# Kernel tuning notes

Hardware: AMD Instinct MI355X
Metric: run time of the kernel (lower is better)

Reference implementation:

```python
import jax, jax.numpy as jnp
import numpy as np

HIDDEN = 4096
NUM_HEADS = 32
NUM_KV_HEADS = 8
HEAD_DIM = HIDDEN // NUM_HEADS  # 128
GROUPS = NUM_HEADS // NUM_KV_HEADS  # 4
ROPE_THETA = 10000.0


def setup_inputs() -> dict:
    key = jax.random.key(0)
    ks = jax.random.split(key, 5)
    B, S = 1, 2048
    w_scale = 0.02
    hidden_states = jax.random.normal(ks[0], (B, S, HIDDEN), dtype=jnp.float32)
    # nn.Linear weights stored as [out_features, in_features] (torch convention)
    Wq = jax.random.normal(ks[1], (NUM_HEADS * HEAD_DIM, HIDDEN), dtype=jnp.float32) * w_scale
    Wk = jax.random.normal(ks[2], (NUM_KV_HEADS * HEAD_DIM, HIDDEN), dtype=jnp.float32) * w_scale
    Wv = jax.random.normal(ks[3], (NUM_KV_HEADS * HEAD_DIM, HIDDEN), dtype=jnp.float32) * w_scale
    Wo = jax.random.normal(ks[4], (HIDDEN, NUM_HEADS * HEAD_DIM), dtype=jnp.float32) * w_scale
    position_ids = jnp.arange(S, dtype=jnp.int32)[None, :]  # [B, S]
    return {"hidden_states": hidden_states, "Wq": Wq, "Wk": Wk, "Wv": Wv,
            "Wo": Wo, "position_ids": position_ids}


def _rotate_half(x):
    h = x.shape[-1] // 2
    return jnp.concatenate([-x[..., h:], x[..., :h]], axis=-1)


def _rope_cos_sin(position_ids, dtype):
    # Llama rotary embedding: inv_freq over even dims, duplicated halves.
    inv_freq = 1.0 / (ROPE_THETA ** (jnp.arange(0, HEAD_DIM, 2, dtype=jnp.float32) / HEAD_DIM))
    freqs = position_ids.astype(jnp.float32)[..., None] * inv_freq  # [B, S, HD/2]
    emb = jnp.concatenate([freqs, freqs], axis=-1)  # [B, S, HD]
    cos = jnp.cos(emb)[:, None].astype(dtype)  # [B, 1, S, HD]
    sin = jnp.sin(emb)[:, None].astype(dtype)
    return cos, sin


def reference(hidden_states, Wq, Wk, Wv, Wo, position_ids):
    B, S, _ = hidden_states.shape
    # q/k/v projections (no bias, attention_bias=False)
    q = (hidden_states @ Wq.T).reshape(B, S, NUM_HEADS, HEAD_DIM).transpose(0, 2, 1, 3)
    k = (hidden_states @ Wk.T).reshape(B, S, NUM_KV_HEADS, HEAD_DIM).transpose(0, 2, 1, 3)
    v = (hidden_states @ Wv.T).reshape(B, S, NUM_KV_HEADS, HEAD_DIM).transpose(0, 2, 1, 3)
    # RoPE
    cos, sin = _rope_cos_sin(position_ids, hidden_states.dtype)
    q = q * cos + _rotate_half(q) * sin
    k = k * cos + _rotate_half(k) * sin
    # repeat_kv for GQA
    k = jnp.repeat(k, GROUPS, axis=1)  # [B, NH, S, HD]
    v = jnp.repeat(v, GROUPS, axis=1)
    # causal scaled dot product attention (matches the module's custom SDPA helper)
    scale = jnp.asarray(1.0 / np.sqrt(HEAD_DIM), hidden_states.dtype)
    scores = jnp.einsum('bhqd,bhkd->bhqk', q, k) * scale
    causal = jnp.tril(jnp.ones((S, S), dtype=bool))
    scores = jnp.where(causal, scores, jnp.asarray(-1e9, scores.dtype))
    attn = jax.nn.softmax(scores, axis=-1)
    out = jnp.einsum('bhqk,bhkd->bhqd', attn, v)  # [B, NH, S, HD]
    out = out.transpose(0, 2, 1, 3).reshape(B, S, NUM_HEADS * HEAD_DIM)
    return out @ Wo.T
```

## Files before the change

### kernel.cpp

```cpp
#include <hip/hip_runtime.h>
#include <hip/hip_fp16.h>

#define S_LEN 2048
#define HID   4096
#define NH    32
#define NKV   8
#define HD    128

using half8 = __attribute__((ext_vector_type(8))) _Float16;
using f32x4 = __attribute__((ext_vector_type(4))) float;

__device__ __forceinline__ void async16(const void* g, void* l) {
  __builtin_amdgcn_global_load_lds(
      (const __attribute__((address_space(1))) unsigned int*)g,
      (__attribute__((address_space(3))) unsigned int*)l, 16, 0, 0);
}

__global__ void k_cvt(const float* __restrict__ in, __half* __restrict__ out, int n) {
  int idx = blockIdx.x * blockDim.x + threadIdx.x;
  int stride = gridDim.x * blockDim.x;
  for (int i = idx * 4; i < n; i += stride * 4) {
    float4 v = *(const float4*)(in + i);
    __half2* o = (__half2*)(out + i);
    o[0] = __floats2half2_rn(v.x, v.y);
    o[1] = __floats2half2_rn(v.z, v.w);
  }
}

__global__ __launch_bounds__(256) void k_gemm(const __half* __restrict__ A,
                                              const __half* __restrict__ B,
                                              __half* __restrict__ Ch,
                                              float* __restrict__ Cf,
                                              int M, int N, int K, int mode) {
  __shared__ __half As[128 * 32];
  __shared__ __half Bs[128 * 32];
  const int tid = threadIdx.x;
  const int lane = tid & 63;
  const int wave = tid >> 6;
  const int m0 = blockIdx.x * 128, n0 = blockIdx.y * 128;
  const int wm = (wave >> 1) * 64, wn = (wave & 1) * 64;
  const int lr = lane & 15, lg = lane >> 4;

  f32x4 acc[4][4];
#pragma unroll
  for (int i = 0; i < 4; ++i)
#pragma unroll
    for (int j = 0; j < 4; ++j) acc[i][j] = f32x4{0.f, 0.f, 0.f, 0.f};

  for (int kt = 0; kt < K; kt += 32) {
    __syncthreads();
#pragma unroll
    for (int q = 0; q < 2; ++q) {
      int chunk = q * 256 + wave * 64 + lane;
      int row = chunk >> 2, kc = chunk & 3;
      async16(A + (size_t)(m0 + row) * K + kt + kc * 8,
              (char*)As + q * 4096 + wave * 1024);
      async16(B + (size_t)(n0 + row) * K + kt + kc * 8,
              (char*)Bs + q * 4096 + wave * 1024);
    }
    __syncthreads();

    half8 af[4], bfr[4];
#pragma unroll
    for (int i = 0; i < 4; ++i) {
      af[i]  = *(const half8*)((const char*)As + (wm + i * 16 + lr) * 64 + lg * 16);
      bfr[i] = *(const half8*)((const char*)Bs + (wn + i * 16 + lr) * 64 + lg * 16);
    }
#pragma unroll
    for (int i = 0; i < 4; ++i)
#pragma unroll
      for (int j = 0; j < 4; ++j)
        acc[i][j] = __builtin_amdgcn_mfma_f32_16x16x32_f16(af[i], bfr[j], acc[i][j], 0, 0, 0);
  }

#pragma unroll
  for (int i = 0; i < 4; ++i)
#pragma unroll
    for (int j = 0; j < 4; ++j) {
      int col = n0 + wn + j * 16 + lr;
#pragma unroll
      for (int r = 0; r < 4; ++r) {
        int row = m0 + wm + i * 16 + lg * 4 + r;
        if (mode == 1)      Cf[(size_t)row * N + col] = acc[i][j][r];
        else if (mode == 2) Ch[(size_t)col * M + row] = __float2half(acc[i][j][r]);
        else                Ch[(size_t)row * N + col] = __float2half(acc[i][j][r]);
      }
    }
}

__global__ void k_rope(__half* __restrict__ Q, __half* __restrict__ Kv,
                       const int* __restrict__ pos) {
  int idx = blockIdx.x * blockDim.x + threadIdx.x;
  int j = idx & 63;
  int hh = (idx >> 6) % (NH + NKV);
  int s = idx / (64 * (NH + NKV));
  float p = (float)pos[s];
  float invf = exp2f(-(float)j * (13.287712379549449f / 64.0f));
  float ang = p * invf;
  float c, sn;
  sincosf(ang, &c, &sn);
  __half* base = (hh < NH) ? (Q + (size_t)s * HID + hh * HD)
                           : (Kv + (size_t)s * (NKV * HD) + (hh - NH) * HD);
  float x0 = __half2float(base[j]);
  float x1 = __half2float(base[j + 64]);
  base[j]      = __float2half(x0 * c + x1 * sn);
  base[j + 64] = __float2half(x1 * c - x0 * sn);
}

__global__ __launch_bounds__(256) void k_attn(const __half* __restrict__ Q,
                                              const __half* __restrict__ K,
                                              const __half* __restrict__ Vt,
                                              __half* __restrict__ O) {
  __shared__ char Ks[64 * 256];
  __shared__ char Vs[128 * 128];
  __shared__ char Ps[4][2048];
  const int tid = threadIdx.x, lane = tid & 63, wave = tid >> 6;
  const int qb = blockIdx.x, h = blockIdx.y;
  const int kvh = h >> 2;
  const int q0 = qb * 64 + wave * 16;
  const int lr = lane & 15, lg = lane >> 4;

  half8 qf[4];
#pragma unroll
  for (int kc = 0; kc < 4; ++kc)
    qf[kc] = *(const half8*)(Q + (size_t)(q0 + lr) * HID + h * HD + kc * 32 + lg * 8);

  float m_r[4], l_r[4];
  f32x4 oa[8];
#pragma unroll
  for (int r = 0; r < 4; ++r) { m_r[r] = -1e30f; l_r[r] = 0.f; }
#pragma unroll
  for (int t8 = 0; t8 < 8; ++t8) oa[t8] = f32x4{0.f, 0.f, 0.f, 0.f};

  const int kv_end = qb * 64 + 64;
  for (int kv0 = 0; kv0 < kv_end; kv0 += 64) {
    __syncthreads();
#pragma unroll
    for (int q = 0; q < 4; ++q) {
      int chunk = q * 256 + tid;
      int row = chunk >> 4, ck = chunk & 15;
      uint4 d = *(const uint4*)(K + (size_t)(kv0 + row) * (NKV * HD) + kvh * HD + ck * 8);
      *(uint4*)(Ks + row * 256 + (((ck ^ (row & 7))) << 4)) = d;
    }
#pragma unroll
    for (int q = 0; q < 4; ++q) {
      int chunk = q * 256 + tid;
      int row = chunk >> 3, ck = chunk & 7;
      uint4 d = *(const uint4*)(Vt + (size_t)(kvh * HD + row) * S_LEN + kv0 + ck * 8);
      *(uint4*)(Vs + row * 128 + (((ck ^ (row & 7))) << 4)) = d;
    }
    __syncthreads();

    f32x4 sc[4];
#pragma unroll
    for (int c = 0; c < 4; ++c) sc[c] = f32x4{0.f, 0.f, 0.f, 0.f};
#pragma unroll
    for (int c = 0; c < 4; ++c) {
      int row = c * 16 + lr;
#pragma unroll
      for (int kc = 0; kc < 4; ++kc) {
        int ck = (kc * 4 + lg) ^ (row & 7);
        half8 kf = *(const half8*)(Ks + row * 256 + ck * 16);
        sc[c] = __builtin_amdgcn_mfma_f32_16x16x32_f16(qf[kc], kf, sc[c], 0, 0, 0);
      }
    }

    float pv[4][4];
#pragma unroll
    for (int c = 0; c < 4; ++c) {
      int kvg = kv0 + c * 16 + lr;
#pragma unroll
      for (int r = 0; r < 4; ++r) {
        int qg = q0 + lg * 4 + r;
        float v = sc[c][r] * 0.08838834764831845f;
        pv[c][r] = (kvg <= qg) ? v : -1e30f;
      }
    }
#pragma unroll
    for (int r = 0; r < 4; ++r) {
      float t = fmaxf(fmaxf(pv[0][r], pv[1][r]), fmaxf(pv[2][r], pv[3][r]));
      t = fmaxf(t, __shfl_xor(t, 1));
      t = fmaxf(t, __shfl_xor(t, 2));
      t = fmaxf(t, __shfl_xor(t, 4));
      t = fmaxf(t, __shfl_xor(t, 8));
      float mnew = fmaxf(m_r[r], t);
      float scal = __expf(m_r[r] - mnew);
      m_r[r] = mnew;
      float ps = 0.f;
#pragma unroll
      for (int c = 0; c < 4; ++c) {
        float p = __expf(pv[c][r] - mnew);
        pv[c][r] = p;
        ps += p;
      }
      ps += __shfl_xor(ps, 1);
      ps += __shfl_xor(ps, 2);
      ps += __shfl_xor(ps, 4);
      ps += __shfl_xor(ps, 8);
      l_r[r] = l_r[r] * scal + ps;
#pragma unroll
      for (int t8 = 0; t8 < 8; ++t8) oa[t8][r] *= scal;
    }

#pragma unroll
    for (int c = 0; c < 4; ++c)
#pragma unroll
      for (int r = 0; r < 4; ++r)
        *(__half*)(Ps[wave] + (lg * 4 + r) * 128 + (c * 16 + lr) * 2) = __float2half(pv[c][r]);
    __syncthreads();
    half8 pa[2];
#pragma unroll
    for (int kc = 0; kc < 2; ++kc)
      pa[kc] = *(const half8*)(Ps[wave] + lr * 128 + kc * 64 + lg * 16);

#pragma unroll
    for (int t8 = 0; t8 < 8; ++t8) {
#pragma unroll
      for (int kc = 0; kc < 2; ++kc) {
        int dd = t8 * 16 + lr;
        int ck = (kc * 4 + lg) ^ (dd & 7);
        half8 vf = *(const half8*)(Vs + dd * 128 + ck * 16);
        oa[t8] = __builtin_amdgcn_mfma_f32_16x16x32_f16(pa[kc], vf, oa[t8], 0, 0, 0);
      }
    }
  }

#pragma unroll
  for (int t8 = 0; t8 < 8; ++t8)
#pragma unroll
    for (int r = 0; r < 4; ++r) {
      float o = oa[t8][r] / l_r[r];
      O[(size_t)(q0 + lg * 4 + r) * HID + h * HD + t8 * 16 + lr] = __float2half(o);
    }
}

extern "C" void kernel_launch(void* const* d_in, const int* in_sizes, int n_in,
                              void* d_out, int out_size, void* d_ws, size_t ws_size,
                              hipStream_t stream) {
  const float* X  = (const float*)d_in[0];
  const float* Wq = (const float*)d_in[1];
  const float* Wk = (const float*)d_in[2];
  const float* Wv = (const float*)d_in[3];
  const float* Wo = (const float*)d_in[4];
  const int* pos  = (const int*)d_in[5];
  char* ws = (char*)d_ws;

  __half* Xh   = (__half*)(ws + 0);
  __half* Wbuf = (__half*)(ws + 16777216);
  __half* Wkh  = (__half*)(ws + 50331648);
  __half* Wvh  = (__half*)(ws + 58720256);
  __half* Qh   = (__half*)(ws + 67108864);
  __half* Kh   = (__half*)(ws + 83886080);
  __half* Vth  = (__half*)(ws + 88080384);
  __half* AOh  = Xh;

  k_cvt<<<2048, 256, 0, stream>>>(X,  Xh,   S_LEN * HID);
  k_cvt<<<2048, 256, 0, stream>>>(Wq, Wbuf, HID * HID);
  k_cvt<<<2048, 256, 0, stream>>>(Wk, Wkh,  NKV * HD * HID);
  k_cvt<<<2048, 256, 0, stream>>>(Wv, Wvh,  NKV * HD * HID);

  k_gemm<<<dim3(16, 32), 256, 0, stream>>>(Xh, Wbuf, Qh, nullptr, S_LEN, HID, HID, 0);
  k_gemm<<<dim3(16, 8),  256, 0, stream>>>(Xh, Wkh,  Kh, nullptr, S_LEN, NKV * HD, HID, 0);
  k_gemm<<<dim3(16, 8),  256, 0, stream>>>(Xh, Wvh,  Vth, nullptr, S_LEN, NKV * HD, HID, 2);

  k_cvt<<<2048, 256, 0, stream>>>(Wo, Wbuf, HID * HID);

  k_rope<<<(S_LEN * (NH + NKV) * 64) / 256, 256, 0, stream>>>(Qh, Kh, pos);

  k_attn<<<dim3(S_LEN / 64, NH), 256, 0, stream>>>(Qh, Kh, Vth, AOh);

  k_gemm<<<dim3(16, 32), 256, 0, stream>>>(AOh, Wbuf, nullptr, (float*)d_out, S_LEN, HID, HID, 1);
}
```

Before: 661.8 us.

## Pair causal query blocks per workgroup and prefetch K/V tiles into registers

The attention kernel now launches half as many workgroups, and each processes two query blocks: one near the end of the sequence and one near the start (31-x and x). This gives every workgroup the same amount of causal work. It also software-pipelines the K/V tile loads: the next tile is read from global memory into registers while the current tile is being computed. The P scratch row stride is padded from 128 to 144 bytes to reduce LDS bank conflicts. In exchange, register pressure rises from holding the prefetched tiles, and there are fewer workgroups to fill the GPU.

```diff
diff --git a/kernel.cpp b/kernel.cpp
--- a/kernel.cpp
+++ b/kernel.cpp
@@ -113,125 +113,146 @@
                                               __half* __restrict__ O) {
   __shared__ char Ks[64 * 256];
   __shared__ char Vs[128 * 128];
-  __shared__ char Ps[4][2048];
+  __shared__ char Ps[4][2304];
   const int tid = threadIdx.x, lane = tid & 63, wave = tid >> 6;
-  const int qb = blockIdx.x, h = blockIdx.y;
+  const int xblk = blockIdx.x, h = blockIdx.y;
   const int kvh = h >> 2;
-  const int q0 = qb * 64 + wave * 16;
   const int lr = lane & 15, lg = lane >> 4;
 
-  half8 qf[4];
-#pragma unroll
-  for (int kc = 0; kc < 4; ++kc)
-    qf[kc] = *(const half8*)(Q + (size_t)(q0 + lr) * HID + h * HD + kc * 32 + lg * 8);
-
-  float m_r[4], l_r[4];
-  f32x4 oa[8];
-#pragma unroll
-  for (int r = 0; r < 4; ++r) { m_r[r] = -1e30f; l_r[r] = 0.f; }
-#pragma unroll
-  for (int t8 = 0; t8 < 8; ++t8) oa[t8] = f32x4{0.f, 0.f, 0.f, 0.f};
-
-  const int kv_end = qb * 64 + 64;
-  for (int kv0 = 0; kv0 < kv_end; kv0 += 64) {
-    __syncthreads();
+  const int r0 = (tid >> 4) & 0;
+
+#pragma unroll
+  for (int seg = 0; seg < 2; ++seg) {
+    const int qb = seg ? xblk : (31 - xblk);
+    const int q0 = qb * 64 + wave * 16;
+    const int kv_end = qb * 64 + 64;
+
+    half8 qf[4];
+#pragma unroll
+    for (int kc = 0; kc < 4; ++kc)
+      qf[kc] = *(const half8*)(Q + (size_t)(q0 + lr) * HID + h * HD + kc * 32 + lg * 8);
+
+    float m_r[4], l_r[4];
+    f32x4 oa[8];
+#pragma unroll
+    for (int r = 0; r < 4; ++r) { m_r[r] = -1e30f; l_r[r] = 0.f; }
+#pragma unroll
+    for (int t8 = 0; t8 < 8; ++t8) oa[t8] = f32x4{0.f, 0.f, 0.f, 0.f};
+
+    uint4 rk[4], rv[4];
 #pragma unroll
     for (int q = 0; q < 4; ++q) {
       int chunk = q * 256 + tid;
       int row = chunk >> 4, ck = chunk & 15;
-      uint4 d = *(const uint4*)(K + (size_t)(kv0 + row) * (NKV * HD) + kvh * HD + ck * 8);
-      *(uint4*)(Ks + row * 256 + (((ck ^ (row & 7))) << 4)) = d;
-    }
-#pragma unroll
-    for (int q = 0; q < 4; ++q) {
-      int chunk = q * 256 + tid;
-      int row = chunk >> 3, ck = chunk & 7;
-      uint4 d = *(const uint4*)(Vt + (size_t)(kvh * HD + row) * S_LEN + kv0 + ck * 8);
-      *(uint4*)(Vs + row * 128 + (((ck ^ (row & 7))) << 4)) = d;
-    }
-    __syncthreads();
-
-    f32x4 sc[4];
-#pragma unroll
-    for (int c = 0; c < 4; ++c) sc[c] = f32x4{0.f, 0.f, 0.f, 0.f};
-#pragma unroll
-    for (int c = 0; c < 4; ++c) {
-      int row = c * 16 + lr;
-#pragma unroll
-      for (int kc = 0; kc < 4; ++kc) {
-        int ck = (kc * 4 + lg) ^ (row & 7);
-        half8 kf = *(const half8*)(Ks + row * 256 + ck * 16);
-        sc[c] = __builtin_amdgcn_mfma_f32_16x16x32_f16(qf[kc], kf, sc[c], 0, 0, 0);
-      }
-    }
-
-    float pv[4][4];
-#pragma unroll
-    for (int c = 0; c < 4; ++c) {
-      int kvg = kv0 + c * 16 + lr;
+      rk[q] = *(const uint4*)(K + (size_t)(0 + row) * (NKV * HD) + kvh * HD + ck * 8);
+      int rowv = chunk >> 3, ckv = chunk & 7;
+      rv[q] = *(const uint4*)(Vt + (size_t)(kvh * HD + rowv) * S_LEN + 0 + ckv * 8);
+    }
+
+    for (int kv0 = 0; kv0 < kv_end; kv0 += 64) {
+      __syncthreads();
+#pragma unroll
+      for (int q = 0; q < 4; ++q) {
+        int chunk = q * 256 + tid;
+        int row = chunk >> 4, ck = chunk & 15;
+        *(uint4*)(Ks + row * 256 + (((ck ^ (row & 7))) << 4)) = rk[q];
+        int rowv = chunk >> 3, ckv = chunk & 7;
+        *(uint4*)(Vs + rowv * 128 + (((ckv ^ (rowv & 7))) << 4)) = rv[q];
+      }
+      __syncthreads();
+      if (kv0 + 64 < kv_end) {
+#pragma unroll
+        for (int q = 0; q < 4; ++q) {
+          int chunk = q * 256 + tid;
+          int row = chunk >> 4, ck = chunk & 15;
+          rk[q] = *(const uint4*)(K + (size_t)(kv0 + 64 + row) * (NKV * HD) + kvh * HD + ck * 8);
+          int rowv = chunk >> 3, ckv = chunk & 7;
+          rv[q] = *(const uint4*)(Vt + (size_t)(kvh * HD + rowv) * S_LEN + kv0 + 64 + ckv * 8);
+        }
+      }
+
+      f32x4 sc[4];
+#pragma unroll
+      for (int c = 0; c < 4; ++c) sc[c] = f32x4{0.f, 0.f, 0.f, 0.f};
+#pragma unroll
+      for (int c = 0; c < 4; ++c) {
+        int row = c * 16 + lr;
+#pragma unroll
+        for (int kc = 0; kc < 4; ++kc) {
+          int ck = (kc * 4 + lg) ^ (row & 7);
+          half8 kf = *(const half8*)(Ks + row * 256 + ck * 16);
+          sc[c] = __builtin_amdgcn_mfma_f32_16x16x32_f16(qf[kc], kf, sc[c], 0, 0, 0);
+        }
+      }
+
+      float pv[4][4];
+#pragma unroll
+      for (int c = 0; c < 4; ++c) {
+        int kvg = kv0 + c * 16 + lr;
+#pragma unroll
+        for (int r = 0; r < 4; ++r) {
+          int qg = q0 + lg * 4 + r;
+          float v = sc[c][r] * 0.08838834764831845f;
+          pv[c][r] = (kvg <= qg) ? v : -1e30f;
+        }
+      }
 #pragma unroll
       for (int r = 0; r < 4; ++r) {
-        int qg = q0 + lg * 4 + r;
-        float v = sc[c][r] * 0.08838834764831845f;
-        pv[c][r] = (kvg <= qg) ? v : -1e30f;
-      }
-    }
-#pragma unroll
-    for (int r = 0; r < 4; ++r) {
-      float t = fmaxf(fmaxf(pv[0][r], pv[1][r]), fmaxf(pv[2][r], pv[3][r]));
-      t = fmaxf(t, __shfl_xor(t, 1));
-      t = fmaxf(t, __shfl_xor(t, 2));
-      t = fmaxf(t, __shfl_xor(t, 4));
-      t = fmaxf(t, __shfl_xor(t, 8));
-      float mnew = fmaxf(m_r[r], t);
-      float scal = __expf(m_r[r] - mnew);
-      m_r[r] = mnew;
-      float ps = 0.f;
-#pragma unroll
-      for (int c = 0; c < 4; ++c) {
-        float p = __expf(pv[c][r] - mnew);
-        pv[c][r] = p;
-        ps += p;
-      }
-      ps += __shfl_xor(ps, 1);
-      ps += __shfl_xor(ps, 2);
-      ps += __shfl_xor(ps, 4);
-      ps += __shfl_xor(ps, 8);
-      l_r[r] = l_r[r] * scal + ps;
-#pragma unroll
-      for (int t8 = 0; t8 < 8; ++t8) oa[t8][r] *= scal;
-    }
-
-#pragma unroll
-    for (int c = 0; c < 4; ++c)
-#pragma unroll
-      for (int r = 0; r < 4; ++r)
-        *(__half*)(Ps[wave] + (lg * 4 + r) * 128 + (c * 16 + lr) * 2) = __float2half(pv[c][r]);
-    __syncthreads();
-    half8 pa[2];
-#pragma unroll
-    for (int kc = 0; kc < 2; ++kc)
-      pa[kc] = *(const half8*)(Ps[wave] + lr * 128 + kc * 64 + lg * 16);
-
-#pragma unroll
-    for (int t8 = 0; t8 < 8; ++t8) {
-#pragma unroll
-      for (int kc = 0; kc < 2; ++kc) {
-        int dd = t8 * 16 + lr;
-        int ck = (kc * 4 + lg) ^ (dd & 7);
-        half8 vf = *(const half8*)(Vs + dd * 128 + ck * 16);
-        oa[t8] = __builtin_amdgcn_mfma_f32_16x16x32_f16(pa[kc], vf, oa[t8], 0, 0, 0);
-      }
-    }
+        float t = fmaxf(fmaxf(pv[0][r], pv[1][r]), fmaxf(pv[2][r], pv[3][r]));
+        t = fmaxf(t, __shfl_xor(t, 1));
+        t = fmaxf(t, __shfl_xor(t, 2));
+        t = fmaxf(t, __shfl_xor(t, 4));
+        t = fmaxf(t, __shfl_xor(t, 8));
+        float mnew = fmaxf(m_r[r], t);
+        float scal = __expf(m_r[r] - mnew);
+        m_r[r] = mnew;
+        float ps = 0.f;
+#pragma unroll
+        for (int c = 0; c < 4; ++c) {
+          float p = __expf(pv[c][r] - mnew);
+          pv[c][r] = p;
+          ps += p;
+        }
+        ps += __shfl_xor(ps, 1);
+        ps += __shfl_xor(ps, 2);
+        ps += __shfl_xor(ps, 4);
+        ps += __shfl_xor(ps, 8);
+        l_r[r] = l_r[r] * scal + ps;
+#pragma unroll
+        for (int t8 = 0; t8 < 8; ++t8) oa[t8][r] *= scal;
+      }
+
+#pragma unroll
+      for (int c = 0; c < 4; ++c)
+#pragma unroll
+        for (int r = 0; r < 4; ++r)
+          *(__half*)(Ps[wave] + (lg * 4 + r) * 144 + (c * 16 + lr) * 2) = __float2half(pv[c][r]);
+      __syncthreads();
+      half8 pa[2];
+#pragma unroll
+      for (int kc = 0; kc < 2; ++kc)
+        pa[kc] = *(const half8*)(Ps[wave] + lr * 144 + kc * 64 + lg * 16);
+
+#pragma unroll
+      for (int t8 = 0; t8 < 8; ++t8) {
+#pragma unroll
+        for (int kc = 0; kc < 2; ++kc) {
+          int dd = t8 * 16 + lr;
+          int ck = (kc * 4 + lg) ^ (dd & 7);
+          half8 vf = *(const half8*)(Vs + dd * 128 + ck * 16);
+          oa[t8] = __builtin_amdgcn_mfma_f32_16x16x32_f16(pa[kc], vf, oa[t8], 0, 0, 0);
+        }
+      }
+    }
+
+#pragma unroll
+    for (int t8 = 0; t8 < 8; ++t8)
+#pragma unroll
+      for (int r = 0; r < 4; ++r) {
+        float o = oa[t8][r] / l_r[r];
+        O[(size_t)(q0 + lg * 4 + r) * HID + h * HD + t8 * 16 + lr] = __float2half(o);
+      }
   }
-
-#pragma unroll
-  for (int t8 = 0; t8 < 8; ++t8)
-#pragma unroll
-    for (int r = 0; r < 4; ++r) {
-      float o = oa[t8][r] / l_r[r];
-      O[(size_t)(q0 + lg * 4 + r) * HID + h * HD + t8 * 16 + lr] = __float2half(o);
-    }
 }
 
 extern "C" void kernel_launch(void* const* d_in, const int* in_sizes, int n_in,
@@ -267,7 +288,7 @@
 
   k_rope<<<(S_LEN * (NH + NKV) * 64) / 256, 256, 0, stream>>>(Qh, Kh, pos);
 
-  k_attn<<<dim3(S_LEN / 64, NH), 256, 0, stream>>>(Qh, Kh, Vth, AOh);
+  k_attn<<<dim3(16, NH), 256, 0, stream>>>(Qh, Kh, Vth, AOh);
 
   k_gemm<<<dim3(16, 32), 256, 0, stream>>>(AOh, Wbuf, nullptr, (float*)d_out, S_LEN, HID, HID, 1);
 }
```

After: 657.2 us. No clear change (-0.7%).
